# Performance work log

Measured on AMD Instinct MI355X. Metric: run time of the kernel, lower is better.

The kernel has to match this reference:

```python
import jax, jax.numpy as jnp
import numpy as np

B, N, F_IN, DEG = 8, 4096, 8, 8
E = B * N * DEG
MAX_RADIUS, NUM_BASIS, HIDDEN = 3.0, 10, 64
MUL0, MUL1 = 32, 16  # irreps_potential = '32x0e + 16x1o'
W_NUMEL = F_IN * (MUL0 + MUL1)  # 384


def setup_inputs() -> dict:
    key = jax.random.key(0)
    k1, k2, k3, k4, k5, k6 = jax.random.split(key, 6)
    node_features = jax.random.normal(k1, (B, N, F_IN), jnp.float32)
    pos = 4.0 * jax.random.uniform(k2, (B, N, 3), dtype=jnp.float32)  # box so many pairs fall inside max_radius
    # static-shape stand-in for radius_graph: DEG random neighbors per node, within each graph, no self loops
    src = jax.random.randint(k3, (B, N * DEG), 0, N)
    off = jax.random.randint(k4, (B, N * DEG), 1, N)
    dst = (src + off) % N
    boff = (jnp.arange(B) * N)[:, None]
    edge_src = (src + boff).reshape(-1).astype(jnp.int32)
    edge_dst = (dst + boff).reshape(-1).astype(jnp.int32)
    W1 = jax.random.normal(k5, (NUM_BASIS, HIDDEN), jnp.float32)
    W2 = jax.random.normal(k6, (HIDDEN, W_NUMEL), jnp.float32)
    return {"node_features": node_features, "pos": pos, "edge_src": edge_src,
            "edge_dst": edge_dst, "W1": W1, "W2": W2}


def _forward(node_features, pos, edge_src, edge_dst, W1, W2):
    pos_flat = pos.reshape(-1, 3)            # [B*N, 3]
    x_flat = node_features.reshape(-1, F_IN)  # [B*N, F_IN]
    edge_vec = pos_flat[edge_src] - pos_flat[edge_dst]  # [E,3]
    r = jnp.sqrt(jnp.sum(edge_vec * edge_vec, axis=1) + 1e-18)  # [E]

    # soft_one_hot_linspace(r, 0, R, num_basis, basis='smooth_finite', cutoff=True) * sqrt(num_basis)
    values = jnp.linspace(0.0, MAX_RADIUS, NUM_BASIS + 2)[1:-1]
    step = values[1] - values[0]
    d = (r[:, None] - values[None, :]) / step
    inside = jnp.abs(d) < 1.0
    y = jnp.where(inside, jnp.maximum(1.0 - d * d, 1e-7), 1.0)
    emb = jnp.where(inside, 1.14136 * jnp.exp(2.0) * jnp.exp(-1.0 / y), 0.0)
    emb = emb * (NUM_BASIS ** 0.5)           # [E, num_basis]

    # soft_unit_step(10 * (1 - r/R))
    t = 10.0 * (1.0 - r / MAX_RADIUS)
    w_cut = jnp.where(t > 0.0, jnp.exp(-1.0 / jnp.where(t > 0.0, t, 1.0)), 0.0)

    # spherical harmonics lmax=2, normalize=True, 'component' normalization
    u = edge_vec / r[:, None]
    ux, uy, uz = u[:, 0], u[:, 1], u[:, 2]
    sh1 = jnp.sqrt(3.0) * u                  # l=1 (component norm); sh0 == 1
    c15 = np.sqrt(15.0)
    sh2 = jnp.stack([c15 * ux * uy, c15 * uy * uz, 0.5 * np.sqrt(5.0) * (3 * uz * uz - 1.0),
                     c15 * ux * uz, 0.5 * c15 * (ux * ux - uy * uy)], axis=1)
    del sh2  # 2e couples 0e input only to 2e, which is absent from '32x0e+16x1o' -> no path

    # FullyConnectedNet([num_basis, hidden, weight_numel], silu) -> per-edge TP weights
    h = jax.nn.silu(emb @ (W1 / np.sqrt(NUM_BASIS)))
    w = h @ (W2 / np.sqrt(HIDDEN))           # [E, 384]
    wA = w[:, : F_IN * MUL0].reshape(-1, F_IN, MUL0)
    wB = w[:, F_IN * MUL0:].reshape(-1, F_IN, MUL1)

    # FullyConnectedTensorProduct (uvw), shared_weights=False, path norm 1/sqrt(fan_in)
    x_src = x_flat[edge_src]                 # gather [E, F_IN]
    inv = 1.0 / np.sqrt(F_IN)
    out0 = jnp.einsum('eu,euw->ew', x_src, wA) * inv            # 0e x 0e -> 32x0e
    out1 = jnp.einsum('eu,ei,euw->ewi', x_src, sh1, wB) * inv   # 0e x 1o -> 16x1o
    potential = jnp.concatenate([out0, out1.reshape(-1, 3 * MUL1)], axis=1)  # [E, 80]

    # scatter-add to destination nodes
    nodes = jax.ops.segment_sum(w_cut[:, None] * potential, edge_dst, num_segments=B * N)
    psi = nodes[:, :3].reshape(B, N, 3)
    curl = jnp.stack([psi[..., 2] - psi[..., 1],
                      psi[..., 0] - psi[..., 2],
                      psi[..., 1] - psi[..., 0]], axis=-1)       # [B, N, 3]
    return curl


def reference(node_features, pos, edge_src, edge_dst, W1, W2):
    return _forward(node_features, pos, edge_src, edge_dst, W1, W2)
```

## Files before the change

### kernel.cpp

```cpp
#include <hip/hip_runtime.h>


#define THREADS 256

__global__ __launch_bounds__(THREADS) void se3_edge_kernel(
    const float* __restrict__ x,
    const float* __restrict__ pos,
    const int*   __restrict__ esrc,
    const int*   __restrict__ edst,
    const float* __restrict__ W1,
    const float* __restrict__ W2,
    float*       __restrict__ out,
    int E)
{
    __shared__ float sW1[10 * 65];
    for (int t = threadIdx.x; t < 640; t += THREADS) {
        int j = t >> 6, k = t & 63;
        sW1[j * 65 + k] = W1[t];
    }
    __syncthreads();

    int e = blockIdx.x * THREADS + threadIdx.x;
    if (e >= E) return;

    int s = esrc[e];
    int d = edst[e];

    float ex = pos[3 * s + 0] - pos[3 * d + 0];
    float ey = pos[3 * s + 1] - pos[3 * d + 1];
    float ez = pos[3 * s + 2] - pos[3 * d + 2];
    float r  = sqrtf(ex * ex + ey * ey + ez * ez + 1e-18f);

    float t10 = 10.0f - (10.0f / 3.0f) * r;
    if (t10 <= 0.0f) return;
    float wcut = __expf(-1.0f / t10);

    const float C0 = 8.43357306907549f;
    float q  = r * (11.0f / 3.0f);
    int   jf = (int)q;
    float da = q - (float)jf;
    float db = da - 1.0f;
    float ya = fmaxf(1.0f - da * da, 1e-7f);
    float yb = fmaxf(1.0f - db * db, 1e-7f);
    int ja = jf - 1;
    int jb = jf;
    float ea = (ja >= 0) ? C0 * __expf(-1.0f / ya) : 0.0f;
    float eb = (jb <= 9) ? C0 * __expf(-1.0f / yb) : 0.0f;
    int jac = ja < 0 ? 0 : ja;
    int jbc = jb > 9 ? 9 : jb;

    const float4* xf = reinterpret_cast<const float4*>(x + 8 * (size_t)s);
    float4 xA = xf[0];
    float4 xB = xf[1];

    const float* w1a = sW1 + jac * 65;
    const float* w1b = sW1 + jbc * 65;

    float a0 = 0.0f, a1 = 0.0f, a2 = 0.0f;
#pragma unroll 8
    for (int k = 0; k < 64; ++k) {
        float pre = ea * w1a[k] + eb * w1b[k];
        float hk = pre * __builtin_amdgcn_rcpf(1.0f + __expf(-pre));
        const float* w2k = W2 + k * 384;
        float g0 = xA.x * w2k[0]   + xA.y * w2k[32]  + xA.z * w2k[64]  + xA.w * w2k[96]
                 + xB.x * w2k[128] + xB.y * w2k[160] + xB.z * w2k[192] + xB.w * w2k[224];
        float g1 = xA.x * w2k[1]   + xA.y * w2k[33]  + xA.z * w2k[65]  + xA.w * w2k[97]
                 + xB.x * w2k[129] + xB.y * w2k[161] + xB.z * w2k[193] + xB.w * w2k[225];
        float g2 = xA.x * w2k[2]   + xA.y * w2k[34]  + xA.z * w2k[66]  + xA.w * w2k[98]
                 + xB.x * w2k[130] + xB.y * w2k[162] + xB.z * w2k[194] + xB.w * w2k[226];
        a0 += hk * g0;
        a1 += hk * g1;
        a2 += hk * g2;
    }

    float sc = wcut * 0.04419417382415922f;
    float p0 = a0 * sc, p1 = a1 * sc, p2 = a2 * sc;

    atomicAdd(out + 3 * d + 0, p2 - p1);
    atomicAdd(out + 3 * d + 1, p0 - p2);
    atomicAdd(out + 3 * d + 2, p1 - p0);
}

extern "C" void kernel_launch(void* const* d_in, const int* in_sizes, int n_in,
                              void* d_out, int out_size, void* d_ws, size_t ws_size,
                              hipStream_t stream) {
    const float* x    = (const float*)d_in[0];
    const float* pos  = (const float*)d_in[1];
    const int*   esrc = (const int*)d_in[2];
    const int*   edst = (const int*)d_in[3];
    const float* W1   = (const float*)d_in[4];
    const float* W2   = (const float*)d_in[5];
    float* out = (float*)d_out;

    int E = in_sizes[2];

    hipMemsetAsync(d_out, 0, (size_t)out_size * sizeof(float), stream);
    int blocks = (E + THREADS - 1) / THREADS;
    se3_edge_kernel<<<blocks, THREADS, 0, stream>>>(x, pos, esrc, edst, W1, W2, out, E);
}
```

Before: 117.7 us.

## Precompute radial weight table and interpolate per edge, spread atomics over copies

The MLP output depends only on r through x, so a small kernel tabulates the contracted W2 columns that feed the first three outputs (24 values per radius) on a fine grid of r. The edge kernel then linearly interpolates this table instead of running the 64-step MLP per edge. Scatter atomics are also spread across up to eight workspace copies, which a final kernel sums. This removes most per-edge arithmetic and W2 reads, but adds a table build, a memset and a reduce pass, plus a small interpolation error.

New measurement: 106.6 us. 1.1x faster.

```diff
diff --git a/kernel.cpp b/kernel.cpp
--- a/kernel.cpp
+++ b/kernel.cpp
@@ -2,16 +2,13 @@
 
 
 #define THREADS 256
+#define TROW 32
 
-__global__ __launch_bounds__(THREADS) void se3_edge_kernel(
-    const float* __restrict__ x,
-    const float* __restrict__ pos,
-    const int*   __restrict__ esrc,
-    const int*   __restrict__ edst,
+__global__ __launch_bounds__(THREADS) void se3_build_table(
     const float* __restrict__ W1,
     const float* __restrict__ W2,
-    float*       __restrict__ out,
-    int E)
+    float* __restrict__ T,
+    int R)
 {
     __shared__ float sW1[10 * 65];
     for (int t = threadIdx.x; t < 640; t += THREADS) {
@@ -20,6 +17,49 @@
     }
     __syncthreads();
 
+    int g = blockIdx.x * THREADS + threadIdx.x;
+    if (g >= R * 24) return;
+    int i = g / 24;
+    int j = g - i * 24;
+    int u = j / 3, c = j - u * 3;
+
+    float r = 3.0f * (float)i / (float)(R - 1);
+
+    const float C0 = 8.43357306907549f;
+    float q  = r * (11.0f / 3.0f);
+    int   jf = (int)q;
+    float da = q - (float)jf;
+    float db = da - 1.0f;
+    float ya = fmaxf(1.0f - da * da, 1e-7f);
+    float yb = fmaxf(1.0f - db * db, 1e-7f);
+    int ja = jf - 1, jb = jf;
+    float ea = (ja >= 0) ? C0 * __expf(-1.0f / ya) : 0.0f;
+    float eb = (jb <= 9) ? C0 * __expf(-1.0f / yb) : 0.0f;
+    int jac = ja < 0 ? 0 : ja;
+    int jbc = jb > 9 ? 9 : jb;
+    const float* w1a = sW1 + jac * 65;
+    const float* w1b = sW1 + jbc * 65;
+    const float* w2  = W2 + u * 32 + c;
+
+    float acc = 0.0f;
+#pragma unroll 8
+    for (int k = 0; k < 64; ++k) {
+        float pre = ea * w1a[k] + eb * w1b[k];
+        float h   = pre / (1.0f + __expf(-pre));
+        acc += h * w2[k * 384];
+    }
+    T[i * TROW + j] = acc;
+}
+
+__global__ __launch_bounds__(THREADS) void se3_edge_kernel(
+    const float* __restrict__ x,
+    const float* __restrict__ pos,
+    const int*   __restrict__ esrc,
+    const int*   __restrict__ edst,
+    const float* __restrict__ T,
+    float*       __restrict__ outbuf,
+    int E, int ncopies, int outN, float rscale, int imax)
+{
     int e = blockIdx.x * THREADS + threadIdx.x;
     if (e >= E) return;
 
@@ -35,50 +75,58 @@
     if (t10 <= 0.0f) return;
     float wcut = __expf(-1.0f / t10);
 
-    const float C0 = 8.43357306907549f;
-    float q  = r * (11.0f / 3.0f);
-    int   jf = (int)q;
-    float da = q - (float)jf;
-    float db = da - 1.0f;
-    float ya = fmaxf(1.0f - da * da, 1e-7f);
-    float yb = fmaxf(1.0f - db * db, 1e-7f);
-    int ja = jf - 1;
-    int jb = jf;
-    float ea = (ja >= 0) ? C0 * __expf(-1.0f / ya) : 0.0f;
-    float eb = (jb <= 9) ? C0 * __expf(-1.0f / yb) : 0.0f;
-    int jac = ja < 0 ? 0 : ja;
-    int jbc = jb > 9 ? 9 : jb;
+    float tq = r * rscale;
+    int   i  = (int)tq;
+    if (i > imax) i = imax;
+    float f  = tq - (float)i;
+
+    const float4* T0 = reinterpret_cast<const float4*>(T + (size_t)i * TROW);
+    float tv0[24], tv1[24];
+#pragma unroll
+    for (int q4 = 0; q4 < 6; ++q4) {
+        float4 v0 = T0[q4];
+        float4 v1 = T0[q4 + (TROW / 4)];
+        tv0[4*q4+0] = v0.x; tv0[4*q4+1] = v0.y; tv0[4*q4+2] = v0.z; tv0[4*q4+3] = v0.w;
+        tv1[4*q4+0] = v1.x; tv1[4*q4+1] = v1.y; tv1[4*q4+2] = v1.z; tv1[4*q4+3] = v1.w;
+    }
 
     const float4* xf = reinterpret_cast<const float4*>(x + 8 * (size_t)s);
     float4 xA = xf[0];
     float4 xB = xf[1];
+    float xs[8] = {xA.x, xA.y, xA.z, xA.w, xB.x, xB.y, xB.z, xB.w};
 
-    const float* w1a = sW1 + jac * 65;
-    const float* w1b = sW1 + jbc * 65;
-
-    float a0 = 0.0f, a1 = 0.0f, a2 = 0.0f;
-#pragma unroll 8
-    for (int k = 0; k < 64; ++k) {
-        float pre = ea * w1a[k] + eb * w1b[k];
-        float hk = pre * __builtin_amdgcn_rcpf(1.0f + __expf(-pre));
-        const float* w2k = W2 + k * 384;
-        float g0 = xA.x * w2k[0]   + xA.y * w2k[32]  + xA.z * w2k[64]  + xA.w * w2k[96]
-                 + xB.x * w2k[128] + xB.y * w2k[160] + xB.z * w2k[192] + xB.w * w2k[224];
-        float g1 = xA.x * w2k[1]   + xA.y * w2k[33]  + xA.z * w2k[65]  + xA.w * w2k[97]
-                 + xB.x * w2k[129] + xB.y * w2k[161] + xB.z * w2k[193] + xB.w * w2k[225];
-        float g2 = xA.x * w2k[2]   + xA.y * w2k[34]  + xA.z * w2k[66]  + xA.w * w2k[98]
-                 + xB.x * w2k[130] + xB.y * w2k[162] + xB.z * w2k[194] + xB.w * w2k[226];
-        a0 += hk * g0;
-        a1 += hk * g1;
-        a2 += hk * g2;
+    float p0 = 0.0f, p1 = 0.0f, p2 = 0.0f;
+#pragma unroll
+    for (int u = 0; u < 8; ++u) {
+        float xu = xs[u];
+        int b = 3 * u;
+        p0 = fmaf(xu, fmaf(f, tv1[b+0] - tv0[b+0], tv0[b+0]), p0);
+        p1 = fmaf(xu, fmaf(f, tv1[b+1] - tv0[b+1], tv0[b+1]), p1);
+        p2 = fmaf(xu, fmaf(f, tv1[b+2] - tv0[b+2], tv0[b+2]), p2);
     }
 
     float sc = wcut * 0.04419417382415922f;
-    float p0 = a0 * sc, p1 = a1 * sc, p2 = a2 * sc;
+    p0 *= sc; p1 *= sc; p2 *= sc;
 
-    atomicAdd(out + 3 * d + 0, p2 - p1);
-    atomicAdd(out + 3 * d + 1, p0 - p2);
-    atomicAdd(out + 3 * d + 2, p1 - p0);
+    float* ob = outbuf + (size_t)(blockIdx.x % ncopies) * outN + 3 * d;
+    atomicAdd(ob + 0, p2 - p1);
+    atomicAdd(ob + 1, p0 - p2);
+    atomicAdd(ob + 2, p1 - p0);
+}
+
+__global__ __launch_bounds__(THREADS) void se3_reduce_kernel(
+    const float* __restrict__ ws, float* __restrict__ out,
+    int outN4, int ncopies)
+{
+    int idx = blockIdx.x * THREADS + threadIdx.x;
+    if (idx >= outN4) return;
+    const float4* w = reinterpret_cast<const float4*>(ws);
+    float4 acc = w[idx];
+    for (int c = 1; c < ncopies; ++c) {
+        float4 v = w[(size_t)c * outN4 + idx];
+        acc.x += v.x; acc.y += v.y; acc.z += v.z; acc.w += v.w;
+    }
+    reinterpret_cast<float4*>(out)[idx] = acc;
 }
 
 extern "C" void kernel_launch(void* const* d_in, const int* in_sizes, int n_in,
@@ -92,9 +140,40 @@
     const float* W2   = (const float*)d_in[5];
     float* out = (float*)d_out;
 
-    int E = in_sizes[2];
+    int E    = in_sizes[2];
+    int outN = out_size;
 
-    hipMemsetAsync(d_out, 0, (size_t)out_size * sizeof(float), stream);
-    int blocks = (E + THREADS - 1) / THREADS;
-    se3_edge_kernel<<<blocks, THREADS, 0, stream>>>(x, pos, esrc, edst, W1, W2, out, E);
+    int R = 2048;
+    while (R > 64 && (size_t)R * TROW * sizeof(float) > ws_size) R >>= 1;
+    size_t tableFloats = (size_t)R * TROW;
+    size_t tableBytes  = tableFloats * sizeof(float);
+
+    int ncopies = 0;
+    if (ws_size >= tableBytes) {
+        size_t rem = ws_size - tableBytes;
+        ncopies = (int)(rem / ((size_t)outN * sizeof(float)));
+        if (ncopies > 8) ncopies = 8;
+    }
+
+    float* T = (float*)d_ws;
+    float rscale = (float)(R - 1) / 3.0f;
+    int   imax   = R - 2;
+
+    int buildBlocks = (R * 24 + THREADS - 1) / THREADS;
+    se3_build_table<<<buildBlocks, THREADS, 0, stream>>>(W1, W2, T, R);
+
+    int edgeBlocks = (E + THREADS - 1) / THREADS;
+    if (ncopies >= 2) {
+        float* copies = T + tableFloats;
+        hipMemsetAsync(copies, 0, (size_t)ncopies * outN * sizeof(float), stream);
+        se3_edge_kernel<<<edgeBlocks, THREADS, 0, stream>>>(
+            x, pos, esrc, edst, T, copies, E, ncopies, outN, rscale, imax);
+        int outN4 = outN / 4;
+        se3_reduce_kernel<<<(outN4 + THREADS - 1) / THREADS, THREADS, 0, stream>>>(
+            copies, out, outN4, ncopies);
+    } else {
+        hipMemsetAsync(out, 0, (size_t)outN * sizeof(float), stream);
+        se3_edge_kernel<<<edgeBlocks, THREADS, 0, stream>>>(
+            x, pos, esrc, edst, T, out, E, 1, outN, rscale, imax);
+    }
 }
```
